# Performance work log

Measured on AMD Instinct MI355X. Metric: run time of the kernel, lower is better.

## Reference

```python
import jax, jax.numpy as jnp
import numpy as np

IN_FEATURES = 2048
OUT_FEATURES = 2048
BATCH = 4096


def setup_inputs() -> dict:
    key = jax.random.key(0)
    kx, kw, kb, kp = jax.random.split(key, 4)
    x = jax.random.normal(kx, (BATCH, IN_FEATURES), dtype=jnp.float32)
    weight = jax.random.normal(kw, (OUT_FEATURES, IN_FEATURES), dtype=jnp.float32)
    bias = jax.random.normal(kb, (OUT_FEATURES,), dtype=jnp.float32)
    # torch uses torch.randperm(in_features) at forward time; we fix a permutation here
    indices = jax.random.permutation(kp, IN_FEATURES).astype(jnp.int64)
    return {"x": x, "weight": weight, "bias": bias, "indices": indices}


def reference(x, weight, bias, indices):
    # Original: (x[:, None, :] * weight)[:, :, indices].sum(dim=2) + bias
    # Summing the permuted reduction axis == contracting the permuted operands;
    # we gather both x and weight along the permutation then do a real GEMM,
    # avoiding the huge [B, out, in] intermediate while keeping identical math.
    xp = x[:, indices]            # [B, in]
    wp = weight[:, indices]       # [out, in]
    return jnp.einsum('bi,oi->bo', xp, wp) + bias[None, :]
```

## Files before the change

### kernel.cpp

```cpp
#include <hip/hip_runtime.h>
#include <hip/hip_bf16.h>

#define M_DIM 4096
#define N_DIM 2048
#define K_DIM 2048

#define BM 128
#define BN 128
#define BK 32
#define NT (K_DIM / BK)
#define A_TILE (BM * BK)
#define B_TILE (BN * BK)

typedef __bf16 bf16x8 __attribute__((ext_vector_type(8)));
typedef float f32x4 __attribute__((ext_vector_type(4)));
typedef unsigned short u16x8 __attribute__((ext_vector_type(8)));

__device__ __forceinline__ unsigned short f32_to_bf16_rne(float f) {
  unsigned int u = __float_as_uint(f);
  u += 0x7fffu + ((u >> 16) & 1u);
  return (unsigned short)(u >> 16);
}

__global__ __launch_bounds__(256) void cvt_both(
    const float* __restrict__ x, const float* __restrict__ w,
    unsigned short* __restrict__ out, int xn8, int totn8) {
  int i = blockIdx.x * 256 + threadIdx.x;
  if (i >= totn8) return;
  const float* src = (i < xn8) ? (x + (size_t)i * 8)
                               : (w + (size_t)(i - xn8) * 8);
  f32x4 a = reinterpret_cast<const f32x4*>(src)[0];
  f32x4 b = reinterpret_cast<const f32x4*>(src)[1];
  u16x8 o;
  o[0] = f32_to_bf16_rne(a[0]); o[1] = f32_to_bf16_rne(a[1]);
  o[2] = f32_to_bf16_rne(a[2]); o[3] = f32_to_bf16_rne(a[3]);
  o[4] = f32_to_bf16_rne(b[0]); o[5] = f32_to_bf16_rne(b[1]);
  o[6] = f32_to_bf16_rne(b[2]); o[7] = f32_to_bf16_rne(b[3]);
  reinterpret_cast<u16x8*>(out)[i] = o;
}

__device__ __forceinline__ void gload_lds16(const unsigned short* g, unsigned short* l) {
  __builtin_amdgcn_global_load_lds(
      (const __attribute__((address_space(1))) unsigned int*)g,
      (__attribute__((address_space(3))) unsigned int*)l, 16, 0, 0);
}

#define LD8(p) (*reinterpret_cast<const bf16x8*>(p))
#define VMWAIT_(n) asm volatile("s_waitcnt vmcnt(" #n ")" ::: "memory")
#define VMWAIT(n) VMWAIT_(n)
#define SBAR() __builtin_amdgcn_s_barrier()
#define SCHED() __builtin_amdgcn_sched_barrier(0)

__global__ __launch_bounds__(256, 2) void gemm_tb(
    const unsigned short* __restrict__ A,
    const unsigned short* __restrict__ B,
    const float* __restrict__ bias,
    float* __restrict__ C) {
  __shared__ unsigned short As[3 * A_TILE];
  __shared__ unsigned short Bs[3 * B_TILE];

  const int tid  = threadIdx.x;
  const int lane = tid & 63;
  const int wave = tid >> 6;
  const int wr   = wave >> 1;
  const int wc   = wave & 1;

  const int orig = blockIdx.x;
  const int xcd  = orig & 7;
  const int idx  = orig >> 3;
  const int bm   = (xcd & 3) * 8 + (idx & 7);
  const int bn   = (xcd >> 2) * 8 + (idx >> 3);

  const int lid  = tid >> 3;
  const int uu   = (tid & 7) ^ (lid & 7);
  const int grow = 2 * lid + (uu >> 2);
  const int kc   = (uu & 3) * 8;
  const unsigned short* Ag[2];
  const unsigned short* Bg[2];
#pragma unroll
  for (int j = 0; j < 2; ++j) {
    Ag[j] = A + (size_t)(bm * BM + j * 64 + grow) * K_DIM + kc;
    Bg[j] = B + (size_t)(bn * BN + j * 64 + grow) * K_DIM + kc;
  }

#define STAGE(bufLit, k0) do { \
    unsigned short* _da = &As[(bufLit) * A_TILE + tid * 8]; \
    unsigned short* _db = &Bs[(bufLit) * B_TILE + tid * 8]; \
    gload_lds16(Ag[0] + (k0), _da); \
    gload_lds16(Ag[1] + (k0), _da + 2048); \
    gload_lds16(Bg[0] + (k0), _db); \
    gload_lds16(Bg[1] + (k0), _db + 2048); \
  } while (0)

  const int fr = lane & 15;
  const int qq = lane >> 4;
  int aoff[4], boff[4];
#pragma unroll
  for (int mi = 0; mi < 4; ++mi) {
    const int R = wr * 64 + mi * 16 + fr;
    aoff[mi] = (R >> 1) * 64 + ((((R & 1) * 4 + qq) ^ ((R >> 1) & 7)) * 8);
  }
#pragma unroll
  for (int ni = 0; ni < 4; ++ni) {
    const int R = wc * 64 + ni * 16 + fr;
    boff[ni] = (R >> 1) * 64 + ((((R & 1) * 4 + qq) ^ ((R >> 1) & 7)) * 8);
  }

  const f32x4 z = {0.f, 0.f, 0.f, 0.f};
  f32x4 acc[4][4];
#pragma unroll
  for (int i = 0; i < 4; ++i)
#pragma unroll
    for (int j = 0; j < 4; ++j) acc[i][j] = z;

  bf16x8 Xa[4], Xb[4], Ya[4], Yb[4];

#define READ_SET(Sa, Sb, bufLit) do { \
    const unsigned short* _a = &As[(bufLit) * A_TILE]; \
    const unsigned short* _b = &Bs[(bufLit) * B_TILE]; \
    Sb[0] = LD8(_b + boff[0]); Sb[1] = LD8(_b + boff[1]); \
    Sb[2] = LD8(_b + boff[2]); Sb[3] = LD8(_b + boff[3]); \
    Sa[0] = LD8(_a + aoff[0]); Sa[1] = LD8(_a + aoff[1]); \
    Sa[2] = LD8(_a + aoff[2]); Sa[3] = LD8(_a + aoff[3]); \
  } while (0)

#define MFMA_SET(Sa, Sb) do { \
    __builtin_amdgcn_s_setprio(1); \
    _Pragma("unroll") \
    for (int mi = 0; mi < 4; ++mi) { \
      acc[mi][0] = __builtin_amdgcn_mfma_f32_16x16x32_bf16(Sa[mi], Sb[0], acc[mi][0], 0, 0, 0); \
      acc[mi][1] = __builtin_amdgcn_mfma_f32_16x16x32_bf16(Sa[mi], Sb[1], acc[mi][1], 0, 0, 0); \
      acc[mi][2] = __builtin_amdgcn_mfma_f32_16x16x32_bf16(Sa[mi], Sb[2], acc[mi][2], 0, 0, 0); \
      acc[mi][3] = __builtin_amdgcn_mfma_f32_16x16x32_bf16(Sa[mi], Sb[3], acc[mi][3], 0, 0, 0); \
    } \
    __builtin_amdgcn_s_setprio(0); \
  } while (0)

#define TILE(stgB, rdB, Scur_a, Scur_b, Snxt_a, Snxt_b, k0) do { \
    STAGE(stgB, k0); \
    MFMA_SET(Scur_a, Scur_b); \
    VMWAIT(4); \
    SBAR(); \
    SCHED(); \
    READ_SET(Snxt_a, Snxt_b, rdB); \
  } while (0)

  STAGE(0, 0);
  STAGE(1, BK);
  VMWAIT(4);
  SBAR();
  SCHED();
  READ_SET(Xa, Xb, 0);

#pragma unroll 1
  for (int s = 0; s < 10; ++s) {
    const int kb = (6 * s + 2) * BK;
    TILE(2, 1, Xa, Xb, Ya, Yb, kb);
    TILE(0, 2, Ya, Yb, Xa, Xb, kb + BK);
    TILE(1, 0, Xa, Xb, Ya, Yb, kb + 2 * BK);
    TILE(2, 1, Ya, Yb, Xa, Xb, kb + 3 * BK);
    TILE(0, 2, Xa, Xb, Ya, Yb, kb + 4 * BK);
    TILE(1, 0, Ya, Yb, Xa, Xb, kb + 5 * BK);
  }

  TILE(2, 1, Xa, Xb, Ya, Yb, 62 * BK);
  TILE(0, 2, Ya, Yb, Xa, Xb, 63 * BK);
  MFMA_SET(Xa, Xb);
  VMWAIT(0);
  SBAR();
  SCHED();
  READ_SET(Ya, Yb, 0);
  MFMA_SET(Ya, Yb);

  const int orow0 = bm * BM + wr * 64 + qq * 4;
  const int ocol0 = bn * BN + wc * 64 + fr;
#pragma unroll
  for (int ni = 0; ni < 4; ++ni) {
    const int col = ocol0 + ni * 16;
    const float bvv = bias[col];
#pragma unroll
    for (int mi = 0; mi < 4; ++mi) {
      const int row = orow0 + mi * 16;
#pragma unroll
      for (int r = 0; r < 4; ++r)
        C[(size_t)(row + r) * N_DIM + col] = acc[mi][ni][r] + bvv;
    }
  }
#undef TILE
#undef MFMA_SET
#undef READ_SET
#undef STAGE
}

__global__ __launch_bounds__(256) void gemm_f32_naive(
    const float* __restrict__ X, const float* __restrict__ W,
    const float* __restrict__ bias, float* __restrict__ C) {
  int o = blockIdx.x * 256 + threadIdx.x;
  if (o >= M_DIM * N_DIM) return;
  int m = o / N_DIM, n = o % N_DIM;
  const float* xr = X + (size_t)m * K_DIM;
  const float* wr = W + (size_t)n * K_DIM;
  float s = 0.f;
  for (int k = 0; k < K_DIM; ++k) s += xr[k] * wr[k];
  C[o] = s + bias[n];
}

extern "C" void kernel_launch(void* const* d_in, const int* in_sizes, int n_in,
                              void* d_out, int out_size, void* d_ws, size_t ws_size,
                              hipStream_t stream) {
  const float* x    = (const float*)d_in[0];
  const float* w    = (const float*)d_in[1];
  const float* bias = (const float*)d_in[2];
  float* out = (float*)d_out;

  const size_t x_elems = (size_t)M_DIM * K_DIM;
  const size_t w_elems = (size_t)N_DIM * K_DIM;
  const size_t need = (x_elems + w_elems) * sizeof(unsigned short);

  if (ws_size < need) {
    gemm_f32_naive<<<(M_DIM * N_DIM + 255) / 256, 256, 0, stream>>>(x, w, bias, out);
    return;
  }

  unsigned short* xb = (unsigned short*)d_ws;
  unsigned short* wb = xb + x_elems;

  const int xn8 = (int)(x_elems / 8);
  const int totn8 = (int)((x_elems + w_elems) / 8);
  cvt_both<<<(totn8 + 255) / 256, 256, 0, stream>>>(x, w, xb, xn8, totn8);

  gemm_tb<<<512, 256, 0, stream>>>(xb, wb, bias, out);
}
```

Measured before the change: 55.71 us.

## Use inline-asm LDS reads with immediate offsets and overlap them with MFMAs

Replaces compiler-generated LDS fragment loads with inline ds_read_b128 using precomputed byte addresses and immediate offsets into a single interleaved A/B buffer. This removes per-tile address arithmetic. It also reorders each tile so the next fragment set is read right after the barrier and runs concurrently with the current MFMAs, followed by an explicit lgkmcnt wait and barrier. The cost is a second barrier per tile and manual waitcnt handling that the compiler can no longer schedule around.

New measurement: 56.75 us. Within noise of the previous version (+1.9%).

```diff
diff --git a/kernel.cpp b/kernel.cpp
--- a/kernel.cpp
+++ b/kernel.cpp
@@ -9,11 +9,11 @@
 #define BN 128
 #define BK 32
 #define NT (K_DIM / BK)
-#define A_TILE (BM * BK)
-#define B_TILE (BN * BK)
+#define BUF_EL 8192
 
 typedef __bf16 bf16x8 __attribute__((ext_vector_type(8)));
 typedef float f32x4 __attribute__((ext_vector_type(4)));
+typedef int   i32x4 __attribute__((ext_vector_type(4)));
 typedef unsigned short u16x8 __attribute__((ext_vector_type(8)));
 
 __device__ __forceinline__ unsigned short f32_to_bf16_rne(float f) {
@@ -45,19 +45,26 @@
       (__attribute__((address_space(3))) unsigned int*)l, 16, 0, 0);
 }
 
-#define LD8(p) (*reinterpret_cast<const bf16x8*>(p))
 #define VMWAIT_(n) asm volatile("s_waitcnt vmcnt(" #n ")" ::: "memory")
 #define VMWAIT(n) VMWAIT_(n)
+#define LGKM0() do { \
+    asm volatile("s_waitcnt lgkmcnt(0)" ::: "memory"); \
+    __builtin_amdgcn_sched_barrier(0); \
+  } while (0)
 #define SBAR() __builtin_amdgcn_s_barrier()
 #define SCHED() __builtin_amdgcn_sched_barrier(0)
 
-__global__ __launch_bounds__(256, 2) void gemm_tb(
+#define DSREAD(dst, addr, OFS) \
+  asm volatile("ds_read_b128 %0, %1 offset:" OFS : "=v"(dst) : "v"(addr))
+
+#define BCAST(v) __builtin_bit_cast(bf16x8, v)
+
+__global__ __launch_bounds__(256, 2) void gemm_asm(
     const unsigned short* __restrict__ A,
     const unsigned short* __restrict__ B,
     const float* __restrict__ bias,
     float* __restrict__ C) {
-  __shared__ unsigned short As[3 * A_TILE];
-  __shared__ unsigned short Bs[3 * B_TILE];
+  __shared__ unsigned short L[3 * BUF_EL];
 
   const int tid  = threadIdx.x;
   const int lane = tid & 63;
@@ -84,8 +91,8 @@
   }
 
 #define STAGE(bufLit, k0) do { \
-    unsigned short* _da = &As[(bufLit) * A_TILE + tid * 8]; \
-    unsigned short* _db = &Bs[(bufLit) * B_TILE + tid * 8]; \
+    unsigned short* _da = &L[(bufLit) * BUF_EL + tid * 8]; \
+    unsigned short* _db = &L[(bufLit) * BUF_EL + 4096 + tid * 8]; \
     gload_lds16(Ag[0] + (k0), _da); \
     gload_lds16(Ag[1] + (k0), _da + 2048); \
     gload_lds16(Bg[0] + (k0), _db); \
@@ -94,16 +101,21 @@
 
   const int fr = lane & 15;
   const int qq = lane >> 4;
-  int aoff[4], boff[4];
-#pragma unroll
-  for (int mi = 0; mi < 4; ++mi) {
-    const int R = wr * 64 + mi * 16 + fr;
-    aoff[mi] = (R >> 1) * 64 + ((((R & 1) * 4 + qq) ^ ((R >> 1) & 7)) * 8);
-  }
-#pragma unroll
-  for (int ni = 0; ni < 4; ++ni) {
-    const int R = wc * 64 + ni * 16 + fr;
-    boff[ni] = (R >> 1) * 64 + ((((R & 1) * 4 + qq) ^ ((R >> 1) & 7)) * 8);
+  unsigned adrA[4], adrB[4];
+  {
+    const unsigned base = (unsigned)(uintptr_t)(&L[0]);
+#pragma unroll
+    for (int mi = 0; mi < 4; ++mi) {
+      const int R = wr * 64 + mi * 16 + fr;
+      const int e = (R >> 1) * 64 + ((((R & 1) * 4 + qq) ^ ((R >> 1) & 7)) * 8);
+      adrA[mi] = base + e * 2;
+    }
+#pragma unroll
+    for (int ni = 0; ni < 4; ++ni) {
+      const int R = wc * 64 + ni * 16 + fr;
+      const int e = (R >> 1) * 64 + ((((R & 1) * 4 + qq) ^ ((R >> 1) & 7)) * 8);
+      adrB[ni] = base + 8192 + e * 2;
+    }
   }
 
   const f32x4 z = {0.f, 0.f, 0.f, 0.f};
@@ -113,36 +125,59 @@
 #pragma unroll
     for (int j = 0; j < 4; ++j) acc[i][j] = z;
 
-  bf16x8 Xa[4], Xb[4], Ya[4], Yb[4];
-
-#define READ_SET(Sa, Sb, bufLit) do { \
-    const unsigned short* _a = &As[(bufLit) * A_TILE]; \
-    const unsigned short* _b = &Bs[(bufLit) * B_TILE]; \
-    Sb[0] = LD8(_b + boff[0]); Sb[1] = LD8(_b + boff[1]); \
-    Sb[2] = LD8(_b + boff[2]); Sb[3] = LD8(_b + boff[3]); \
-    Sa[0] = LD8(_a + aoff[0]); Sa[1] = LD8(_a + aoff[1]); \
-    Sa[2] = LD8(_a + aoff[2]); Sa[3] = LD8(_a + aoff[3]); \
-  } while (0)
-
-#define MFMA_SET(Sa, Sb) do { \
+  i32x4 Xa0, Xa1, Xa2, Xa3, Xb0, Xb1, Xb2, Xb3;
+  i32x4 Ya0, Ya1, Ya2, Ya3, Yb0, Yb1, Yb2, Yb3;
+
+#define READ_X(OFS) do { \
+    DSREAD(Xb0, adrB[0], OFS); DSREAD(Xb1, adrB[1], OFS); \
+    DSREAD(Xb2, adrB[2], OFS); DSREAD(Xb3, adrB[3], OFS); \
+    DSREAD(Xa0, adrA[0], OFS); DSREAD(Xa1, adrA[1], OFS); \
+    DSREAD(Xa2, adrA[2], OFS); DSREAD(Xa3, adrA[3], OFS); \
+  } while (0)
+#define READ_Y(OFS) do { \
+    DSREAD(Yb0, adrB[0], OFS); DSREAD(Yb1, adrB[1], OFS); \
+    DSREAD(Yb2, adrB[2], OFS); DSREAD(Yb3, adrB[3], OFS); \
+    DSREAD(Ya0, adrA[0], OFS); DSREAD(Ya1, adrA[1], OFS); \
+    DSREAD(Ya2, adrA[2], OFS); DSREAD(Ya3, adrA[3], OFS); \
+  } while (0)
+
+#define MFMA_ROW(a_, b0_, b1_, b2_, b3_, mi) do { \
+    acc[mi][0] = __builtin_amdgcn_mfma_f32_16x16x32_bf16(BCAST(a_), BCAST(b0_), acc[mi][0], 0, 0, 0); \
+    acc[mi][1] = __builtin_amdgcn_mfma_f32_16x16x32_bf16(BCAST(a_), BCAST(b1_), acc[mi][1], 0, 0, 0); \
+    acc[mi][2] = __builtin_amdgcn_mfma_f32_16x16x32_bf16(BCAST(a_), BCAST(b2_), acc[mi][2], 0, 0, 0); \
+    acc[mi][3] = __builtin_amdgcn_mfma_f32_16x16x32_bf16(BCAST(a_), BCAST(b3_), acc[mi][3], 0, 0, 0); \
+  } while (0)
+
+#define MFMA_X() do { \
     __builtin_amdgcn_s_setprio(1); \
-    _Pragma("unroll") \
-    for (int mi = 0; mi < 4; ++mi) { \
-      acc[mi][0] = __builtin_amdgcn_mfma_f32_16x16x32_bf16(Sa[mi], Sb[0], acc[mi][0], 0, 0, 0); \
-      acc[mi][1] = __builtin_amdgcn_mfma_f32_16x16x32_bf16(Sa[mi], Sb[1], acc[mi][1], 0, 0, 0); \
-      acc[mi][2] = __builtin_amdgcn_mfma_f32_16x16x32_bf16(Sa[mi], Sb[2], acc[mi][2], 0, 0, 0); \
-      acc[mi][3] = __builtin_amdgcn_mfma_f32_16x16x32_bf16(Sa[mi], Sb[3], acc[mi][3], 0, 0, 0); \
-    } \
+    MFMA_ROW(Xa0, Xb0, Xb1, Xb2, Xb3, 0); \
+    MFMA_ROW(Xa1, Xb0, Xb1, Xb2, Xb3, 1); \
+    MFMA_ROW(Xa2, Xb0, Xb1, Xb2, Xb3, 2); \
+    MFMA_ROW(Xa3, Xb0, Xb1, Xb2, Xb3, 3); \
     __builtin_amdgcn_s_setprio(0); \
   } while (0)
-
-#define TILE(stgB, rdB, Scur_a, Scur_b, Snxt_a, Snxt_b, k0) do { \
-    STAGE(stgB, k0); \
-    MFMA_SET(Scur_a, Scur_b); \
-    VMWAIT(4); \
+#define MFMA_Y() do { \
+    __builtin_amdgcn_s_setprio(1); \
+    MFMA_ROW(Ya0, Yb0, Yb1, Yb2, Yb3, 0); \
+    MFMA_ROW(Ya1, Yb0, Yb1, Yb2, Yb3, 1); \
+    MFMA_ROW(Ya2, Yb0, Yb1, Yb2, Yb3, 2); \
+    MFMA_ROW(Ya3, Yb0, Yb1, Yb2, Yb3, 3); \
+    __builtin_amdgcn_s_setprio(0); \
+  } while (0)
+
+#define TILE_X(stgB, OFSRD, k0) do { \
+    STAGE(stgB, k0); VMWAIT(4); SBAR(); SCHED(); \
+    READ_Y(OFSRD); SCHED(); \
+    MFMA_X(); \
+    LGKM0(); \
     SBAR(); \
-    SCHED(); \
-    READ_SET(Snxt_a, Snxt_b, rdB); \
+  } while (0)
+#define TILE_Y(stgB, OFSRD, k0) do { \
+    STAGE(stgB, k0); VMWAIT(4); SBAR(); SCHED(); \
+    READ_X(OFSRD); SCHED(); \
+    MFMA_Y(); \
+    LGKM0(); \
+    SBAR(); \
   } while (0)
 
   STAGE(0, 0);
@@ -150,27 +185,30 @@
   VMWAIT(4);
   SBAR();
   SCHED();
-  READ_SET(Xa, Xb, 0);
+  READ_X("0");
+  LGKM0();
 
 #pragma unroll 1
   for (int s = 0; s < 10; ++s) {
     const int kb = (6 * s + 2) * BK;
-    TILE(2, 1, Xa, Xb, Ya, Yb, kb);
-    TILE(0, 2, Ya, Yb, Xa, Xb, kb + BK);
-    TILE(1, 0, Xa, Xb, Ya, Yb, kb + 2 * BK);
-    TILE(2, 1, Ya, Yb, Xa, Xb, kb + 3 * BK);
-    TILE(0, 2, Xa, Xb, Ya, Yb, kb + 4 * BK);
-    TILE(1, 0, Ya, Yb, Xa, Xb, kb + 5 * BK);
-  }
-
-  TILE(2, 1, Xa, Xb, Ya, Yb, 62 * BK);
-  TILE(0, 2, Ya, Yb, Xa, Xb, 63 * BK);
-  MFMA_SET(Xa, Xb);
+    TILE_X(2, "16384", kb);
+    TILE_Y(0, "32768", kb + BK);
+    TILE_X(1, "0",     kb + 2 * BK);
+    TILE_Y(2, "16384", kb + 3 * BK);
+    TILE_X(0, "32768", kb + 4 * BK);
+    TILE_Y(1, "0",     kb + 5 * BK);
+  }
+
+  TILE_X(2, "16384", 62 * BK);
+  TILE_Y(0, "32768", 63 * BK);
   VMWAIT(0);
   SBAR();
   SCHED();
-  READ_SET(Ya, Yb, 0);
-  MFMA_SET(Ya, Yb);
+  READ_Y("0");
+  SCHED();
+  MFMA_X();
+  LGKM0();
+  MFMA_Y();
 
   const int orow0 = bm * BM + wr * 64 + qq * 4;
   const int ocol0 = bn * BN + wc * 64 + fr;
@@ -186,9 +224,13 @@
         C[(size_t)(row + r) * N_DIM + col] = acc[mi][ni][r] + bvv;
     }
   }
-#undef TILE
-#undef MFMA_SET
-#undef READ_SET
+#undef TILE_X
+#undef TILE_Y
+#undef MFMA_X
+#undef MFMA_Y
+#undef MFMA_ROW
+#undef READ_X
+#undef READ_Y
 #undef STAGE
 }
 
@@ -229,5 +271,5 @@
   const int totn8 = (int)((x_elems + w_elems) / 8);
   cvt_both<<<(totn8 + 255) / 256, 256, 0, stream>>>(x, w, xb, xn8, totn8);
 
-  gemm_tb<<<512, 256, 0, stream>>>(xb, wb, bias, out);
-}
+  gemm_asm<<<512, 256, 0, stream>>>(xb, wb, bias, out);
+}
```
